# Performance work log

Measured on AMD Instinct MI355X. Metric: run time of the kernel, lower is better.

## Reference

```python
import jax, jax.numpy as jnp
import numpy as np

NUM_MID = 10   # hard-coded num_mid_nodes in HiPool.__init__
NUM_HIGH = 5   # ceil(10 / 2)


def map_low_to_high(num_low, num_high):
    # eye(num_high) repeat_interleaved by ceil(low/high) rows, truncated to num_low
    # == one-hot of i // edges_per_high
    edges_per_high = -(-num_low // num_high)
    return jax.nn.one_hot(jnp.arange(num_low) // edges_per_high, num_high,
                          dtype=jnp.float32)  # [low, high]


def cluster_attention(x, mapping, att):
    # x: [s, d], mapping: [s, m], att: [d, d]
    mid = mapping.T @ x                              # [m, d]
    scores = (mid @ att) @ x.T                       # [m, s]
    scores = scores * (1.0 - mapping).T              # zero (not -inf) own-cluster entries, as in source
    scores = jax.nn.softmax(scores, axis=1)
    return scores @ x + mid                          # [m, d]


def dense_gcn(x, adj, W, b):
    # torch_geometric DenseGCNConv with add_loop=True
    n = adj.shape[0]
    i = jnp.arange(n)
    adj = adj.at[i, i].set(1.0)
    deg = jnp.clip(jnp.sum(adj, axis=-1), 1.0, None) ** -0.5
    adj = deg[:, None] * adj * deg[None, :]
    return adj @ (x @ W) + b


def setup_inputs() -> dict:
    key = jax.random.key(0)
    ks = jax.random.split(key, 8)
    S, D, H = 8192, 768, 768
    return {
        "x": jax.random.normal(ks[0], (S, D), dtype=jnp.float32),
        "adjacency_matrix": jax.random.uniform(ks[1], (S, S), dtype=jnp.float32),
        "att_low_mid": jax.random.normal(ks[2], (D, D), dtype=jnp.float32) * 0.04,  # xavier_normal-ish
        "conv1_w": jax.random.normal(ks[3], (D, H), dtype=jnp.float32) * 0.04,
        "conv1_b": jnp.zeros((H,), dtype=jnp.float32),
        "att_mid_high": jax.random.normal(ks[4], (H, H), dtype=jnp.float32) * 0.04,
        "conv2_w": jax.random.normal(ks[5], (H, H), dtype=jnp.float32) * 0.04,
        "conv2_b": jnp.zeros((H,), dtype=jnp.float32),
    }


def reference(x, adjacency_matrix, att_low_mid, conv1_w, conv1_b,
              att_mid_high, conv2_w, conv2_b):
    s = x.shape[0]
    m1 = map_low_to_high(s, NUM_MID)                         # [s, 10]
    mid_adj = m1.T @ adjacency_matrix @ m1                   # [10, 10]
    mid_rep = cluster_attention(x, m1, att_low_mid)          # [10, d]
    x_mid = jax.nn.relu(dense_gcn(mid_rep, mid_adj, conv1_w, conv1_b))
    # F.dropout(...)[0]: dropout treated as identity (eval); [0] just dropped the batch dim
    m2 = map_low_to_high(NUM_MID, NUM_HIGH)                  # [10, 5]
    high_adj = m2.T @ mid_adj @ m2                           # [5, 5]
    high_rep = cluster_attention(x_mid, m2, att_mid_high)    # [5, h]
    out = jax.nn.relu(dense_gcn(high_rep, high_adj, conv2_w, conv2_b))
    return out.mean(axis=0)                                  # [h]
```

## Files before the change

kernel.cpp:

```cpp
#include <hip/hip_runtime.h>

constexpr int S    = 8192;
constexpr int D    = 768;
constexpr int NMID = 10;
constexpr int EPH  = 820;

constexpr int OFF_MADJ = 0;
constexpr int OFF_MID  = 128;
constexpr int OFF_MATT = OFF_MID  + 7680;
constexpr int OFF_Y1   = OFF_MATT + 7680;
constexpr int OFF_Z2   = OFF_Y1   + 7680;
constexpr int OFF_Y2   = OFF_Z2   + 3840;
constexpr int ZERO_END = OFF_Y2   + 3840;
constexpr int OFF_MREP = ZERO_END;
constexpr int OFF_SC   = OFF_MREP + 7680;
constexpr int OFF_XMID = OFF_SC   + 81920;
constexpr int OFF_MID2 = OFF_XMID + 7680;
constexpr int OFF_OUT2 = OFF_MID2 + 3840;
constexpr int OFF_NM   = OFF_OUT2 + 3840;
constexpr int OFF_NH   = OFF_NM   + 100;


__global__ __launch_bounds__(256) void k_zero(float* ws) {
    for (int i = blockIdx.x * 256 + threadIdx.x; i < ZERO_END; i += 32 * 256)
        ws[i] = 0.f;
}

__global__ __launch_bounds__(256) void k_bigpass(const float* __restrict__ A,
                                                 const float* __restrict__ x,
                                                 float* __restrict__ ws) {
    __shared__ float red[256];
    int bx = blockIdx.x;
    if (bx < 800) {
        int p = bx >> 3, sp = bx & 7;
        int i = p / 10, j = p % 10;
        int r0 = i * EPH, r1 = min(r0 + EPH, S);
        int c0 = j * EPH, c1 = min(c0 + EPH, S);
        int nr = r1 - r0;
        int rs0 = r0 + (nr * sp) / 8, rs1 = r0 + (nr * (sp + 1)) / 8;
        int nc4 = (c1 - c0) >> 2;
        float acc = 0.f;
        for (int r = rs0; r < rs1; ++r) {
            const float4* row = (const float4*)(A + (size_t)r * S + c0);
            for (int t = threadIdx.x; t < nc4; t += 256) {
                float4 v = row[t];
                acc += (v.x + v.y) + (v.z + v.w);
            }
        }
        red[threadIdx.x] = acc;
        __syncthreads();
        for (int off = 128; off > 0; off >>= 1) {
            if (threadIdx.x < off) red[threadIdx.x] += red[threadIdx.x + off];
            __syncthreads();
        }
        if (threadIdx.x == 0) atomicAdd(&ws[OFF_MADJ + i * 10 + j], red[0]);
    } else {
        int b  = bx - 800;
        int cl = b / 48;
        int rem = b % 48;
        int cc = rem / 16, sp = rem % 16;
        int r0 = cl * EPH, r1 = min(r0 + EPH, S);
        int nr = r1 - r0;
        int rs0 = r0 + (nr * sp) / 16, rs1 = r0 + (nr * (sp + 1)) / 16;
        int c = cc * 256 + threadIdx.x;
        float acc = 0.f;
        for (int r = rs0; r < rs1; ++r) acc += x[(size_t)r * D + c];
        atomicAdd(&ws[OFF_MID + cl * D + c], acc);
    }
}

__global__ __launch_bounds__(256) void k_copy(float* ws) {
    for (int i = blockIdx.x * 256 + threadIdx.x; i < NMID * D; i += 8 * 256)
        ws[OFF_MREP + i] = ws[OFF_MID + i];
}

template <int NR>
__global__ __launch_bounds__(256) void k_mm(const float* __restrict__ W,
                                            const float* __restrict__ in,
                                            float* __restrict__ out) {
    __shared__ float mi[NR * 16];
    int kb = blockIdx.x * 16;
    for (int t = threadIdx.x; t < NR * 16; t += 256)
        mi[t] = in[(t >> 4) * D + kb + (t & 15)];
    __syncthreads();
    int c = threadIdx.x;
    float a0[NR], a1[NR], a2[NR];
#pragma unroll
    for (int i = 0; i < NR; ++i) { a0[i] = 0.f; a1[i] = 0.f; a2[i] = 0.f; }
    for (int kk = 0; kk < 16; ++kk) {
        const float* wr = W + (size_t)(kb + kk) * D;
        float w0 = wr[c], w1 = wr[c + 256], w2 = wr[c + 512];
#pragma unroll
        for (int i = 0; i < NR; ++i) {
            float m = mi[i * 16 + kk];
            a0[i] += m * w0; a1[i] += m * w1; a2[i] += m * w2;
        }
    }
#pragma unroll
    for (int i = 0; i < NR; ++i) {
        atomicAdd(&out[i * D + c],       a0[i]);
        atomicAdd(&out[i * D + c + 256], a1[i]);
        atomicAdd(&out[i * D + c + 512], a2[i]);
    }
}

__global__ __launch_bounds__(256) void k_scores(const float* __restrict__ x,
                                                float* __restrict__ ws) {
    __shared__ float ma[NMID * D];
    for (int t = threadIdx.x; t < NMID * D; t += 256) ma[t] = ws[OFF_MATT + t];
    __syncthreads();
    const float4* maf = (const float4*)ma;
    const float4* x4  = (const float4*)x;
    int wave = threadIdx.x >> 6, ln = threadIdx.x & 63;
    int rbase = blockIdx.x * 32 + wave * 8;
    for (int rr = 0; rr < 8; ++rr) {
        int r = rbase + rr;
        float4 v0 = x4[(size_t)r * 192 + ln];
        float4 v1 = x4[(size_t)r * 192 + 64 + ln];
        float4 v2 = x4[(size_t)r * 192 + 128 + ln];
        int rc = r / EPH;
#pragma unroll
        for (int i = 0; i < NMID; ++i) {
            float4 m0 = maf[i * 192 + ln];
            float4 m1 = maf[i * 192 + 64 + ln];
            float4 m2 = maf[i * 192 + 128 + ln];
            float p = m0.x * v0.x + m0.y * v0.y + m0.z * v0.z + m0.w * v0.w
                    + m1.x * v1.x + m1.y * v1.y + m1.z * v1.z + m1.w * v1.w
                    + m2.x * v2.x + m2.y * v2.y + m2.z * v2.z + m2.w * v2.w;
#pragma unroll
            for (int off = 32; off > 0; off >>= 1) p += __shfl_down(p, off, 64);
            if (ln == 0) ws[OFF_SC + r * NMID + i] = (rc == i) ? 0.f : p;
        }
    }
}

__global__ __launch_bounds__(256) void k_softmax(float* __restrict__ ws) {
    __shared__ float red[256];
    int i = blockIdx.x;
    if (i < NMID) {
        int tid = threadIdx.x;
        float m = -1e30f;
        for (int r = tid; r < S; r += 256) m = fmaxf(m, ws[OFF_SC + r * NMID + i]);
        red[tid] = m; __syncthreads();
        for (int off = 128; off > 0; off >>= 1) {
            if (tid < off) red[tid] = fmaxf(red[tid], red[tid + off]);
            __syncthreads();
        }
        float M = red[0]; __syncthreads();
        float s = 0.f;
        for (int r = tid; r < S; r += 256) s += expf(ws[OFF_SC + r * NMID + i] - M);
        red[tid] = s; __syncthreads();
        for (int off = 128; off > 0; off >>= 1) {
            if (tid < off) red[tid] += red[tid + off];
            __syncthreads();
        }
        float inv = 1.f / red[0]; __syncthreads();
        for (int r = tid; r < S; r += 256) {
            int idx = OFF_SC + r * NMID + i;
            ws[idx] = expf(ws[idx] - M) * inv;
        }
    } else if (threadIdx.x == 0) {
        float aa[100];
#pragma unroll
        for (int t = 0; t < 100; ++t) aa[t] = ws[OFF_MADJ + t];
        float dg[10];
#pragma unroll
        for (int r = 0; r < 10; ++r) {
            float sum = 0.f;
#pragma unroll
            for (int j = 0; j < 10; ++j) sum += (r == j) ? 1.0f : aa[r * 10 + j];
            dg[r] = 1.0f / sqrtf(fmaxf(sum, 1.0f));
        }
#pragma unroll
        for (int r = 0; r < 10; ++r)
#pragma unroll
            for (int j = 0; j < 10; ++j)
                ws[OFF_NM + r * 10 + j] = dg[r] * ((r == j) ? 1.0f : aa[r * 10 + j]) * dg[j];
        float ha[25];
#pragma unroll
        for (int a = 0; a < 5; ++a)
#pragma unroll
            for (int b = 0; b < 5; ++b)
                ha[a * 5 + b] = aa[(2 * a) * 10 + 2 * b] + aa[(2 * a) * 10 + 2 * b + 1]
                              + aa[(2 * a + 1) * 10 + 2 * b] + aa[(2 * a + 1) * 10 + 2 * b + 1];
        float dh[5];
#pragma unroll
        for (int r = 0; r < 5; ++r) {
            float sum = 0.f;
#pragma unroll
            for (int j = 0; j < 5; ++j) sum += (r == j) ? 1.0f : ha[r * 5 + j];
            dh[r] = 1.0f / sqrtf(fmaxf(sum, 1.0f));
        }
#pragma unroll
        for (int r = 0; r < 5; ++r)
#pragma unroll
            for (int j = 0; j < 5; ++j)
                ws[OFF_NH + r * 5 + j] = dh[r] * ((r == j) ? 1.0f : ha[r * 5 + j]) * dh[j];
    }
}

__global__ __launch_bounds__(192) void k_pv(const float* __restrict__ x,
                                            float* __restrict__ ws) {
    __shared__ float p[64 * NMID];
    int r0 = blockIdx.x * 64;
    int tid = threadIdx.x;
    for (int t = tid; t < 64 * NMID; t += 192) p[t] = ws[OFF_SC + r0 * NMID + t];
    __syncthreads();
    const float4* x4 = (const float4*)x;
    float4 acc[NMID];
#pragma unroll
    for (int i = 0; i < NMID; ++i) acc[i] = make_float4(0.f, 0.f, 0.f, 0.f);
    for (int r = 0; r < 64; ++r) {
        float4 xv = x4[(size_t)(r0 + r) * 192 + tid];
#pragma unroll
        for (int i = 0; i < NMID; ++i) {
            float pv = p[r * NMID + i];
            acc[i].x += pv * xv.x; acc[i].y += pv * xv.y;
            acc[i].z += pv * xv.z; acc[i].w += pv * xv.w;
        }
    }
#pragma unroll
    for (int i = 0; i < NMID; ++i) {
        float* base = ws + OFF_MREP + i * D + tid * 4;
        atomicAdd(base + 0, acc[i].x);
        atomicAdd(base + 1, acc[i].y);
        atomicAdd(base + 2, acc[i].z);
        atomicAdd(base + 3, acc[i].w);
    }
}

__global__ __launch_bounds__(768) void k_xmid(const float* __restrict__ b1,
                                              float* __restrict__ ws) {
    __shared__ float nm[100];
    for (int t = threadIdx.x; t < 100; t += 768) nm[t] = ws[OFF_NM + t];
    __syncthreads();
    int c = threadIdx.x;
    float yv[10];
#pragma unroll
    for (int j = 0; j < 10; ++j) yv[j] = ws[OFF_Y1 + j * D + c];
    float bias = b1[c];
    float xm[10];
#pragma unroll
    for (int i = 0; i < 10; ++i) {
        float s = bias;
#pragma unroll
        for (int j = 0; j < 10; ++j) s += nm[i * 10 + j] * yv[j];
        xm[i] = fmaxf(s, 0.f);
        ws[OFF_XMID + i * D + c] = xm[i];
    }
#pragma unroll
    for (int a = 0; a < 5; ++a)
        ws[OFF_MID2 + a * D + c] = xm[2 * a] + xm[2 * a + 1];
}

__global__ __launch_bounds__(768) void k_attn2(float* __restrict__ ws) {
    __shared__ float s2[64];
    int tid = threadIdx.x;
    int wv = tid >> 6, ln = tid & 63;
    for (int p = wv; p < 50; p += 12) {
        int i = p / 10, r = p % 10;
        const float4* za = (const float4*)(ws + OFF_Z2 + i * D);
        const float4* xa = (const float4*)(ws + OFF_XMID + r * D);
        float acc = 0.f;
#pragma unroll
        for (int q = 0; q < 3; ++q) {
            float4 a = za[q * 64 + ln], b = xa[q * 64 + ln];
            acc += a.x * b.x + a.y * b.y + a.z * b.z + a.w * b.w;
        }
#pragma unroll
        for (int off = 32; off > 0; off >>= 1) acc += __shfl_down(acc, off, 64);
        if (ln == 0) s2[p] = ((r >> 1) == i) ? 0.f : acc;
    }
    __syncthreads();
    if (tid < 5) {
        float mx = -1e30f;
#pragma unroll
        for (int r = 0; r < 10; ++r) mx = fmaxf(mx, s2[tid * 10 + r]);
        float sm = 0.f; float e[10];
#pragma unroll
        for (int r = 0; r < 10; ++r) { e[r] = expf(s2[tid * 10 + r] - mx); sm += e[r]; }
#pragma unroll
        for (int r = 0; r < 10; ++r) s2[tid * 10 + r] = e[r] / sm;
    }
    __syncthreads();
    int c = tid;
    float o[5];
#pragma unroll
    for (int i = 0; i < 5; ++i) o[i] = ws[OFF_MID2 + i * D + c];
#pragma unroll
    for (int r = 0; r < 10; ++r) {
        float xv = ws[OFF_XMID + r * D + c];
#pragma unroll
        for (int i = 0; i < 5; ++i) o[i] += s2[i * 10 + r] * xv;
    }
#pragma unroll
    for (int i = 0; i < 5; ++i) ws[OFF_OUT2 + i * D + c] = o[i];
}

__global__ __launch_bounds__(768) void k_final(const float* __restrict__ b2,
                                               const float* __restrict__ ws,
                                               float* __restrict__ out) {
    __shared__ float nh[25];
    for (int t = threadIdx.x; t < 25; t += 768) nh[t] = ws[OFF_NH + t];
    __syncthreads();
    int c = threadIdx.x;
    float y[5];
#pragma unroll
    for (int j = 0; j < 5; ++j) y[j] = ws[OFF_Y2 + j * D + c];
    float bias = b2[c];
    float s = 0.f;
#pragma unroll
    for (int i = 0; i < 5; ++i) {
        float v = bias;
#pragma unroll
        for (int j = 0; j < 5; ++j) v += nh[i * 5 + j] * y[j];
        s += fmaxf(v, 0.f);
    }
    out[c] = s * 0.2f;
}

extern "C" void kernel_launch(void* const* d_in, const int* in_sizes, int n_in,
                              void* d_out, int out_size, void* d_ws, size_t ws_size,
                              hipStream_t stream) {
    const float* x    = (const float*)d_in[0];
    const float* adj  = (const float*)d_in[1];
    const float* attL = (const float*)d_in[2];
    const float* W1   = (const float*)d_in[3];
    const float* b1   = (const float*)d_in[4];
    const float* attH = (const float*)d_in[5];
    const float* W2   = (const float*)d_in[6];
    const float* b2   = (const float*)d_in[7];
    float* ws  = (float*)d_ws;
    float* out = (float*)d_out;

    k_zero   <<<32,   256, 0, stream>>>(ws);
    k_bigpass<<<1280, 256, 0, stream>>>(adj, x, ws);
    k_copy   <<<8,    256, 0, stream>>>(ws);
    k_mm<10> <<<48,   256, 0, stream>>>(attL, ws + OFF_MID,  ws + OFF_MATT);
    k_scores <<<256,  256, 0, stream>>>(x, ws);
    k_softmax<<<11,   256, 0, stream>>>(ws);
    k_pv     <<<128,  192, 0, stream>>>(x, ws);
    k_mm<10> <<<48,   256, 0, stream>>>(W1, ws + OFF_MREP, ws + OFF_Y1);
    k_xmid   <<<1,    768, 0, stream>>>(b1, ws);
    k_mm<5>  <<<48,   256, 0, stream>>>(attH, ws + OFF_MID2, ws + OFF_Z2);
    k_attn2  <<<1,    768, 0, stream>>>(ws);
    k_mm<5>  <<<48,   256, 0, stream>>>(W2, ws + OFF_OUT2, ws + OFF_Y2);
    k_final  <<<1,    768, 0, stream>>>(b2, ws, out);
}
```

Measured before the change: 185.9 us.

## Fuse pipeline stages into fewer launches with partial-sum buffers and split softmax

Cuts the pipeline from thirteen launches to eight. The zeroing kernel is folded into the big pass, which now writes per-block partial sums instead of atomics, and later kernels finish those reductions. The softmax becomes a two-level online max/sum: each scores block records its local max and sum, and the PV kernel combines them. The small serial single-block stages (adjacency normalization, xmid, attn2) are folded into the prologues of the matmul kernels. This removes launch overhead and serialized single-block work, but every matmul block now recomputes the small normalization and the PV blocks redo the global softmax reduction.

```diff
diff --git a/kernel.cpp b/kernel.cpp
--- a/kernel.cpp
+++ b/kernel.cpp
@@ -5,33 +5,52 @@
 constexpr int NMID = 10;
 constexpr int EPH  = 820;
 
-constexpr int OFF_MADJ = 0;
-constexpr int OFF_MID  = 128;
-constexpr int OFF_MATT = OFF_MID  + 7680;
-constexpr int OFF_Y1   = OFF_MATT + 7680;
-constexpr int OFF_Z2   = OFF_Y1   + 7680;
-constexpr int OFF_Y2   = OFF_Z2   + 3840;
-constexpr int ZERO_END = OFF_Y2   + 3840;
-constexpr int OFF_MREP = ZERO_END;
-constexpr int OFF_SC   = OFF_MREP + 7680;
-constexpr int OFF_XMID = OFF_SC   + 81920;
-constexpr int OFF_MID2 = OFF_XMID + 7680;
-constexpr int OFF_OUT2 = OFF_MID2 + 3840;
-constexpr int OFF_NM   = OFF_OUT2 + 3840;
-constexpr int OFF_NH   = OFF_NM   + 100;
-
-
-__global__ __launch_bounds__(256) void k_zero(float* ws) {
-    for (int i = blockIdx.x * 256 + threadIdx.x; i < ZERO_END; i += 32 * 256)
-        ws[i] = 0.f;
-}
-
-__global__ __launch_bounds__(256) void k_bigpass(const float* __restrict__ A,
-                                                 const float* __restrict__ x,
-                                                 float* __restrict__ ws) {
-    __shared__ float red[256];
+constexpr int PART_ADJ = 0;
+constexpr int PART_MID = 1024;
+constexpr int OFF_ZB   = 123904;
+constexpr int OFF_MATT = 123904;
+constexpr int OFF_MREP = 131584;
+constexpr int OFF_Y1   = 139264;
+constexpr int OFF_Z2   = 146944;
+constexpr int OFF_Y2   = 150784;
+constexpr int ZERO_N   = 30720;
+constexpr int OFF_MID  = 154624;
+constexpr int OFF_XMID = 162304;
+constexpr int OFF_SC   = 169984;
+constexpr int OFF_SCB  = 251904;
+
+template <int NR>
+__device__ __forceinline__ void mm_core(const float* __restrict__ W,
+                                        const float* mi,
+                                        float* __restrict__ out, int kb) {
+    int c = threadIdx.x;
+    float a0[NR], a1[NR], a2[NR];
+#pragma unroll
+    for (int i = 0; i < NR; ++i) { a0[i] = 0.f; a1[i] = 0.f; a2[i] = 0.f; }
+    for (int kk = 0; kk < 16; ++kk) {
+        const float* wr = W + (size_t)(kb + kk) * D;
+        float w0 = wr[c], w1 = wr[c + 256], w2 = wr[c + 512];
+#pragma unroll
+        for (int i = 0; i < NR; ++i) {
+            float m = mi[i * 16 + kk];
+            a0[i] += m * w0; a1[i] += m * w1; a2[i] += m * w2;
+        }
+    }
+#pragma unroll
+    for (int i = 0; i < NR; ++i) {
+        atomicAdd(&out[i * D + c],       a0[i]);
+        atomicAdd(&out[i * D + c + 256], a1[i]);
+        atomicAdd(&out[i * D + c + 512], a2[i]);
+    }
+}
+
+__global__ __launch_bounds__(256) void k_big(const float* __restrict__ A,
+                                             const float* __restrict__ x,
+                                             float* __restrict__ ws) {
     int bx = blockIdx.x;
+    int tid = threadIdx.x;
     if (bx < 800) {
+        __shared__ float red[256];
         int p = bx >> 3, sp = bx & 7;
         int i = p / 10, j = p % 10;
         int r0 = i * EPH, r1 = min(r0 + EPH, S);
@@ -42,19 +61,19 @@
         float acc = 0.f;
         for (int r = rs0; r < rs1; ++r) {
             const float4* row = (const float4*)(A + (size_t)r * S + c0);
-            for (int t = threadIdx.x; t < nc4; t += 256) {
+            for (int t = tid; t < nc4; t += 256) {
                 float4 v = row[t];
                 acc += (v.x + v.y) + (v.z + v.w);
             }
         }
-        red[threadIdx.x] = acc;
+        red[tid] = acc;
         __syncthreads();
         for (int off = 128; off > 0; off >>= 1) {
-            if (threadIdx.x < off) red[threadIdx.x] += red[threadIdx.x + off];
+            if (tid < off) red[tid] += red[tid + off];
             __syncthreads();
         }
-        if (threadIdx.x == 0) atomicAdd(&ws[OFF_MADJ + i * 10 + j], red[0]);
-    } else {
+        if (tid == 0) ws[PART_ADJ + bx] = red[0];
+    } else if (bx < 1280) {
         int b  = bx - 800;
         int cl = b / 48;
         int rem = b % 48;
@@ -62,56 +81,45 @@
         int r0 = cl * EPH, r1 = min(r0 + EPH, S);
         int nr = r1 - r0;
         int rs0 = r0 + (nr * sp) / 16, rs1 = r0 + (nr * (sp + 1)) / 16;
-        int c = cc * 256 + threadIdx.x;
+        int c = cc * 256 + tid;
         float acc = 0.f;
         for (int r = rs0; r < rs1; ++r) acc += x[(size_t)r * D + c];
-        atomicAdd(&ws[OFF_MID + cl * D + c], acc);
-    }
-}
-
-__global__ __launch_bounds__(256) void k_copy(float* ws) {
-    for (int i = blockIdx.x * 256 + threadIdx.x; i < NMID * D; i += 8 * 256)
-        ws[OFF_MREP + i] = ws[OFF_MID + i];
-}
-
-template <int NR>
-__global__ __launch_bounds__(256) void k_mm(const float* __restrict__ W,
-                                            const float* __restrict__ in,
-                                            float* __restrict__ out) {
-    __shared__ float mi[NR * 16];
+        ws[PART_MID + (sp * NMID + cl) * D + c] = acc;
+    } else {
+        int b = bx - 1280;
+        for (int t = b * 256 + tid; t < ZERO_N; t += 16 * 256)
+            ws[OFF_ZB + t] = 0.f;
+    }
+}
+
+__global__ __launch_bounds__(256) void k_mmA(const float* __restrict__ attL,
+                                             float* __restrict__ ws) {
+    __shared__ float mi[160];
     int kb = blockIdx.x * 16;
-    for (int t = threadIdx.x; t < NR * 16; t += 256)
-        mi[t] = in[(t >> 4) * D + kb + (t & 15)];
-    __syncthreads();
-    int c = threadIdx.x;
-    float a0[NR], a1[NR], a2[NR];
-#pragma unroll
-    for (int i = 0; i < NR; ++i) { a0[i] = 0.f; a1[i] = 0.f; a2[i] = 0.f; }
-    for (int kk = 0; kk < 16; ++kk) {
-        const float* wr = W + (size_t)(kb + kk) * D;
-        float w0 = wr[c], w1 = wr[c + 256], w2 = wr[c + 512];
-#pragma unroll
-        for (int i = 0; i < NR; ++i) {
-            float m = mi[i * 16 + kk];
-            a0[i] += m * w0; a1[i] += m * w1; a2[i] += m * w2;
-        }
-    }
-#pragma unroll
-    for (int i = 0; i < NR; ++i) {
-        atomicAdd(&out[i * D + c],       a0[i]);
-        atomicAdd(&out[i * D + c + 256], a1[i]);
-        atomicAdd(&out[i * D + c + 512], a2[i]);
-    }
+    int tid = threadIdx.x;
+    if (tid < 160) {
+        int cl = tid >> 4, k = tid & 15;
+        float s = 0.f;
+#pragma unroll
+        for (int sp = 0; sp < 16; ++sp)
+            s += ws[PART_MID + (sp * NMID + cl) * D + kb + k];
+        mi[tid] = s;
+        ws[OFF_MID + cl * D + kb + k] = s;
+    }
+    __syncthreads();
+    mm_core<10>(attL, mi, ws + OFF_MATT, kb);
 }
 
 __global__ __launch_bounds__(256) void k_scores(const float* __restrict__ x,
                                                 float* __restrict__ ws) {
     __shared__ float ma[NMID * D];
-    for (int t = threadIdx.x; t < NMID * D; t += 256) ma[t] = ws[OFF_MATT + t];
+    __shared__ float scl[32 * NMID];
+    int tid = threadIdx.x;
+    for (int t = tid; t < NMID * D; t += 256) ma[t] = ws[OFF_MATT + t];
     __syncthreads();
     const float4* maf = (const float4*)ma;
     const float4* x4  = (const float4*)x;
-    int wave = threadIdx.x >> 6, ln = threadIdx.x & 63;
+    int wave = tid >> 6, ln = tid & 63;
     int rbase = blockIdx.x * 32 + wave * 8;
     for (int rr = 0; rr < 8; ++rr) {
         int r = rbase + rr;
@@ -129,82 +137,53 @@
                     + m2.x * v2.x + m2.y * v2.y + m2.z * v2.z + m2.w * v2.w;
 #pragma unroll
             for (int off = 32; off > 0; off >>= 1) p += __shfl_down(p, off, 64);
-            if (ln == 0) ws[OFF_SC + r * NMID + i] = (rc == i) ? 0.f : p;
-        }
-    }
-}
-
-__global__ __launch_bounds__(256) void k_softmax(float* __restrict__ ws) {
-    __shared__ float red[256];
-    int i = blockIdx.x;
-    if (i < NMID) {
-        int tid = threadIdx.x;
+            if (ln == 0) {
+                float v = (rc == i) ? 0.f : p;
+                ws[OFF_SC + r * NMID + i] = v;
+                scl[(wave * 8 + rr) * NMID + i] = v;
+            }
+        }
+    }
+    __syncthreads();
+    if (tid < NMID) {
         float m = -1e30f;
-        for (int r = tid; r < S; r += 256) m = fmaxf(m, ws[OFF_SC + r * NMID + i]);
-        red[tid] = m; __syncthreads();
-        for (int off = 128; off > 0; off >>= 1) {
-            if (tid < off) red[tid] = fmaxf(red[tid], red[tid + off]);
-            __syncthreads();
-        }
-        float M = red[0]; __syncthreads();
-        float s = 0.f;
-        for (int r = tid; r < S; r += 256) s += expf(ws[OFF_SC + r * NMID + i] - M);
-        red[tid] = s; __syncthreads();
-        for (int off = 128; off > 0; off >>= 1) {
-            if (tid < off) red[tid] += red[tid + off];
-            __syncthreads();
-        }
-        float inv = 1.f / red[0]; __syncthreads();
-        for (int r = tid; r < S; r += 256) {
-            int idx = OFF_SC + r * NMID + i;
-            ws[idx] = expf(ws[idx] - M) * inv;
-        }
-    } else if (threadIdx.x == 0) {
-        float aa[100];
-#pragma unroll
-        for (int t = 0; t < 100; ++t) aa[t] = ws[OFF_MADJ + t];
-        float dg[10];
-#pragma unroll
-        for (int r = 0; r < 10; ++r) {
-            float sum = 0.f;
-#pragma unroll
-            for (int j = 0; j < 10; ++j) sum += (r == j) ? 1.0f : aa[r * 10 + j];
-            dg[r] = 1.0f / sqrtf(fmaxf(sum, 1.0f));
-        }
-#pragma unroll
-        for (int r = 0; r < 10; ++r)
-#pragma unroll
-            for (int j = 0; j < 10; ++j)
-                ws[OFF_NM + r * 10 + j] = dg[r] * ((r == j) ? 1.0f : aa[r * 10 + j]) * dg[j];
-        float ha[25];
-#pragma unroll
-        for (int a = 0; a < 5; ++a)
-#pragma unroll
-            for (int b = 0; b < 5; ++b)
-                ha[a * 5 + b] = aa[(2 * a) * 10 + 2 * b] + aa[(2 * a) * 10 + 2 * b + 1]
-                              + aa[(2 * a + 1) * 10 + 2 * b] + aa[(2 * a + 1) * 10 + 2 * b + 1];
-        float dh[5];
-#pragma unroll
-        for (int r = 0; r < 5; ++r) {
-            float sum = 0.f;
-#pragma unroll
-            for (int j = 0; j < 5; ++j) sum += (r == j) ? 1.0f : ha[r * 5 + j];
-            dh[r] = 1.0f / sqrtf(fmaxf(sum, 1.0f));
-        }
-#pragma unroll
-        for (int r = 0; r < 5; ++r)
-#pragma unroll
-            for (int j = 0; j < 5; ++j)
-                ws[OFF_NH + r * 5 + j] = dh[r] * ((r == j) ? 1.0f : ha[r * 5 + j]) * dh[j];
+        for (int r = 0; r < 32; ++r) m = fmaxf(m, scl[r * NMID + tid]);
+        float s = 0.f;
+        for (int r = 0; r < 32; ++r) s += expf(scl[r * NMID + tid] - m);
+        ws[OFF_SCB + blockIdx.x * 20 + tid * 2]     = m;
+        ws[OFF_SCB + blockIdx.x * 20 + tid * 2 + 1] = s;
     }
 }
 
 __global__ __launch_bounds__(192) void k_pv(const float* __restrict__ x,
                                             float* __restrict__ ws) {
-    __shared__ float p[64 * NMID];
+    __shared__ float lm[160], ls[160], Mi[10], Inv[10], p[64 * NMID];
+    int tid = threadIdx.x;
+    if (tid < 160) {
+        int i = tid >> 4, seg = tid & 15;
+        float m = -1e30f;
+        for (int b = seg * 16; b < seg * 16 + 16; ++b)
+            m = fmaxf(m, ws[OFF_SCB + b * 20 + i * 2]);
+        float s = 0.f;
+        for (int b = seg * 16; b < seg * 16 + 16; ++b)
+            s += ws[OFF_SCB + b * 20 + i * 2 + 1] *
+                 expf(ws[OFF_SCB + b * 20 + i * 2] - m);
+        lm[tid] = m; ls[tid] = s;
+    }
+    __syncthreads();
+    if (tid < NMID) {
+        float M = -1e30f;
+        for (int g = 0; g < 16; ++g) M = fmaxf(M, lm[tid * 16 + g]);
+        float Ssum = 0.f;
+        for (int g = 0; g < 16; ++g) Ssum += ls[tid * 16 + g] * expf(lm[tid * 16 + g] - M);
+        Mi[tid] = M; Inv[tid] = 1.f / Ssum;
+    }
+    __syncthreads();
     int r0 = blockIdx.x * 64;
-    int tid = threadIdx.x;
-    for (int t = tid; t < 64 * NMID; t += 192) p[t] = ws[OFF_SC + r0 * NMID + t];
+    for (int t = tid; t < 64 * NMID; t += 192) {
+        int i = t % NMID;
+        p[t] = expf(ws[OFF_SC + r0 * NMID + t] - Mi[i]) * Inv[i];
+    }
     __syncthreads();
     const float4* x4 = (const float4*)x;
     float4 acc[NMID];
@@ -229,36 +208,68 @@
     }
 }
 
-__global__ __launch_bounds__(768) void k_xmid(const float* __restrict__ b1,
-                                              float* __restrict__ ws) {
-    __shared__ float nm[100];
-    for (int t = threadIdx.x; t < 100; t += 768) nm[t] = ws[OFF_NM + t];
-    __syncthreads();
-    int c = threadIdx.x;
-    float yv[10];
-#pragma unroll
-    for (int j = 0; j < 10; ++j) yv[j] = ws[OFF_Y1 + j * D + c];
-    float bias = b1[c];
-    float xm[10];
-#pragma unroll
-    for (int i = 0; i < 10; ++i) {
-        float s = bias;
-#pragma unroll
-        for (int j = 0; j < 10; ++j) s += nm[i * 10 + j] * yv[j];
-        xm[i] = fmaxf(s, 0.f);
-        ws[OFF_XMID + i * D + c] = xm[i];
-    }
-#pragma unroll
-    for (int a = 0; a < 5; ++a)
-        ws[OFF_MID2 + a * D + c] = xm[2 * a] + xm[2 * a + 1];
-}
-
-__global__ __launch_bounds__(768) void k_attn2(float* __restrict__ ws) {
-    __shared__ float s2[64];
-    int tid = threadIdx.x;
-    int wv = tid >> 6, ln = tid & 63;
-    for (int p = wv; p < 50; p += 12) {
-        int i = p / 10, r = p % 10;
+__global__ __launch_bounds__(256) void k_mmB(const float* __restrict__ W1,
+                                             float* __restrict__ ws) {
+    __shared__ float mi[160];
+    int kb = blockIdx.x * 16;
+    int tid = threadIdx.x;
+    if (tid < 160) {
+        int cl = tid >> 4, k = tid & 15;
+        mi[tid] = ws[OFF_MID + cl * D + kb + k] + ws[OFF_MREP + cl * D + kb + k];
+    }
+    __syncthreads();
+    mm_core<10>(W1, mi, ws + OFF_Y1, kb);
+}
+
+__global__ __launch_bounds__(256) void k_mmC(const float* __restrict__ attH,
+                                             const float* __restrict__ b1,
+                                             float* __restrict__ ws) {
+    __shared__ float aa[100], dg[10], NM[100], xml[160], mi[80];
+    int tid = threadIdx.x;
+    if (tid < 100) {
+        float s = 0.f;
+#pragma unroll
+        for (int sp = 0; sp < 8; ++sp) s += ws[PART_ADJ + tid * 8 + sp];
+        aa[tid] = s;
+    }
+    __syncthreads();
+    if (tid < 10) {
+        float s = 0.f;
+#pragma unroll
+        for (int j = 0; j < 10; ++j) s += (tid == j) ? 1.0f : aa[tid * 10 + j];
+        dg[tid] = 1.0f / sqrtf(fmaxf(s, 1.0f));
+    }
+    __syncthreads();
+    if (tid < 100) {
+        int i = tid / 10, j = tid % 10;
+        NM[tid] = dg[i] * ((i == j) ? 1.0f : aa[tid]) * dg[j];
+    }
+    __syncthreads();
+    int kb = blockIdx.x * 16;
+    if (tid < 160) {
+        int i = tid >> 4, c = kb + (tid & 15);
+        float s = b1[c];
+#pragma unroll
+        for (int j = 0; j < 10; ++j) s += NM[i * 10 + j] * ws[OFF_Y1 + j * D + c];
+        float xm = fmaxf(s, 0.f);
+        ws[OFF_XMID + i * D + c] = xm;
+        xml[tid] = xm;
+    }
+    __syncthreads();
+    if (tid < 80) {
+        int a = tid >> 4, k = tid & 15;
+        mi[tid] = xml[(2 * a) * 16 + k] + xml[(2 * a + 1) * 16 + k];
+    }
+    __syncthreads();
+    mm_core<5>(attH, mi, ws + OFF_Z2, kb);
+}
+
+__global__ __launch_bounds__(256) void k_mmD(const float* __restrict__ W2,
+                                             float* __restrict__ ws) {
+    __shared__ float s2[64], P2[50], mi[80];
+    int tid = threadIdx.x, wv = tid >> 6, ln = tid & 63;
+    for (int pp = wv; pp < 50; pp += 4) {
+        int i = pp / 10, r = pp % 10;
         const float4* za = (const float4*)(ws + OFF_Z2 + i * D);
         const float4* xa = (const float4*)(ws + OFF_XMID + r * D);
         float acc = 0.f;
@@ -269,7 +280,7 @@
         }
 #pragma unroll
         for (int off = 32; off > 0; off >>= 1) acc += __shfl_down(acc, off, 64);
-        if (ln == 0) s2[p] = ((r >> 1) == i) ? 0.f : acc;
+        if (ln == 0) s2[pp] = ((r >> 1) == i) ? 0.f : acc;
     }
     __syncthreads();
     if (tid < 5) {
@@ -280,30 +291,55 @@
 #pragma unroll
         for (int r = 0; r < 10; ++r) { e[r] = expf(s2[tid * 10 + r] - mx); sm += e[r]; }
 #pragma unroll
-        for (int r = 0; r < 10; ++r) s2[tid * 10 + r] = e[r] / sm;
-    }
-    __syncthreads();
-    int c = tid;
-    float o[5];
-#pragma unroll
-    for (int i = 0; i < 5; ++i) o[i] = ws[OFF_MID2 + i * D + c];
-#pragma unroll
-    for (int r = 0; r < 10; ++r) {
-        float xv = ws[OFF_XMID + r * D + c];
-#pragma unroll
-        for (int i = 0; i < 5; ++i) o[i] += s2[i * 10 + r] * xv;
-    }
-#pragma unroll
-    for (int i = 0; i < 5; ++i) ws[OFF_OUT2 + i * D + c] = o[i];
+        for (int r = 0; r < 10; ++r) P2[tid * 10 + r] = e[r] / sm;
+    }
+    __syncthreads();
+    int kb = blockIdx.x * 16;
+    if (tid < 80) {
+        int i = tid >> 4, c = kb + (tid & 15);
+        float xm[10];
+#pragma unroll
+        for (int r = 0; r < 10; ++r) xm[r] = ws[OFF_XMID + r * D + c];
+        float o = xm[2 * i] + xm[2 * i + 1];
+#pragma unroll
+        for (int r = 0; r < 10; ++r) o += P2[i * 10 + r] * xm[r];
+        mi[tid] = o;
+    }
+    __syncthreads();
+    mm_core<5>(W2, mi, ws + OFF_Y2, kb);
 }
 
 __global__ __launch_bounds__(768) void k_final(const float* __restrict__ b2,
                                                const float* __restrict__ ws,
                                                float* __restrict__ out) {
-    __shared__ float nh[25];
-    for (int t = threadIdx.x; t < 25; t += 768) nh[t] = ws[OFF_NH + t];
-    __syncthreads();
-    int c = threadIdx.x;
+    __shared__ float aa[100], ha[25], dh[5], NH[25];
+    int tid = threadIdx.x;
+    if (tid < 100) {
+        float s = 0.f;
+#pragma unroll
+        for (int sp = 0; sp < 8; ++sp) s += ws[PART_ADJ + tid * 8 + sp];
+        aa[tid] = s;
+    }
+    __syncthreads();
+    if (tid < 25) {
+        int a = tid / 5, b = tid % 5;
+        ha[tid] = aa[(2 * a) * 10 + 2 * b] + aa[(2 * a) * 10 + 2 * b + 1]
+                + aa[(2 * a + 1) * 10 + 2 * b] + aa[(2 * a + 1) * 10 + 2 * b + 1];
+    }
+    __syncthreads();
+    if (tid < 5) {
+        float s = 0.f;
+#pragma unroll
+        for (int j = 0; j < 5; ++j) s += (tid == j) ? 1.0f : ha[tid * 5 + j];
+        dh[tid] = 1.0f / sqrtf(fmaxf(s, 1.0f));
+    }
+    __syncthreads();
+    if (tid < 25) {
+        int i = tid / 5, j = tid % 5;
+        NH[tid] = dh[i] * ((i == j) ? 1.0f : ha[tid]) * dh[j];
+    }
+    __syncthreads();
+    int c = tid;
     float y[5];
 #pragma unroll
     for (int j = 0; j < 5; ++j) y[j] = ws[OFF_Y2 + j * D + c];
@@ -313,7 +349,7 @@
     for (int i = 0; i < 5; ++i) {
         float v = bias;
 #pragma unroll
-        for (int j = 0; j < 5; ++j) v += nh[i * 5 + j] * y[j];
+        for (int j = 0; j < 5; ++j) v += NH[i * 5 + j] * y[j];
         s += fmaxf(v, 0.f);
     }
     out[c] = s * 0.2f;
@@ -333,17 +369,12 @@
     float* ws  = (float*)d_ws;
     float* out = (float*)d_out;
 
-    k_zero   <<<32,   256, 0, stream>>>(ws);
-    k_bigpass<<<1280, 256, 0, stream>>>(adj, x, ws);
-    k_copy   <<<8,    256, 0, stream>>>(ws);
-    k_mm<10> <<<48,   256, 0, stream>>>(attL, ws + OFF_MID,  ws + OFF_MATT);
-    k_scores <<<256,  256, 0, stream>>>(x, ws);
-    k_softmax<<<11,   256, 0, stream>>>(ws);
-    k_pv     <<<128,  192, 0, stream>>>(x, ws);
-    k_mm<10> <<<48,   256, 0, stream>>>(W1, ws + OFF_MREP, ws + OFF_Y1);
-    k_xmid   <<<1,    768, 0, stream>>>(b1, ws);
-    k_mm<5>  <<<48,   256, 0, stream>>>(attH, ws + OFF_MID2, ws + OFF_Z2);
-    k_attn2  <<<1,    768, 0, stream>>>(ws);
-    k_mm<5>  <<<48,   256, 0, stream>>>(W2, ws + OFF_OUT2, ws + OFF_Y2);
-    k_final  <<<1,    768, 0, stream>>>(b2, ws, out);
-}
+    k_big   <<<1296, 256, 0, stream>>>(adj, x, ws);
+    k_mmA   <<<48,   256, 0, stream>>>(attL, ws);
+    k_scores<<<256,  256, 0, stream>>>(x, ws);
+    k_pv    <<<128,  192, 0, stream>>>(x, ws);
+    k_mmB   <<<48,   256, 0, stream>>>(W1, ws);
+    k_mmC   <<<48,   256, 0, stream>>>(attH, b1, ws);
+    k_mmD   <<<48,   256, 0, stream>>>(W2, ws);
+    k_final <<<1,    768, 0, stream>>>(b2, ws, out);
+}
```

New measurement: 165.9 us. 10.8% less time.
